# Kernel tuning notes

Measured on AMD Instinct MI355X. Metric: run time of the kernel, lower is better.

Reference implementation:

```python
import jax, jax.numpy as jnp
import numpy as np

B, S, H = 32, 4096, 768   # tuples, seq len, longformer hidden
N = 2048                  # total signals across all tuples (segments)
T = 16384                 # total pooled token indices (flattened ragged lists)
C = 32                    # char_size side features
D1, D2 = 512, 512         # MLP hidden dims


def setup_inputs() -> dict:
    key = jax.random.key(0)
    ks = jax.random.split(key, 9)
    hidden_states = jax.random.normal(ks[0], (B, S, H), dtype=jnp.float32)
    base_characteristics = jax.random.normal(ks[1], (N, C), dtype=jnp.float32)
    # MLP params: Linear(768+C,512) -> ReLU -> Linear(512,512) -> ReLU -> Linear(512,1) -> Sigmoid
    w1 = jax.random.normal(ks[2], (H + C, D1), dtype=jnp.float32) * 0.02
    b1 = jnp.zeros((D1,), dtype=jnp.float32)
    w2 = jax.random.normal(ks[3], (D1, D2), dtype=jnp.float32) * 0.02
    b2 = jnp.zeros((D2,), dtype=jnp.float32)
    w3 = jax.random.normal(ks[4], (D2, 1), dtype=jnp.float32) * 0.02
    b3 = jnp.zeros((1,), dtype=jnp.float32)
    # Flattened ragged pooling indices: token_indices index into flattened [B*S] tokens,
    # segment_ids map each index to its (tuple, signal) segment in [0, N).
    token_indices = jax.random.randint(ks[5], (T,), 0, B * S, dtype=jnp.int64)
    segment_ids = jnp.sort(jax.random.randint(ks[6], (T,), 0, N, dtype=jnp.int64))
    return {
        "hidden_states": hidden_states,
        "base_characteristics": base_characteristics,
        "w1": w1, "b1": b1, "w2": w2, "b2": b2, "w3": w3, "b3": b3,
        "token_indices": token_indices,
        "segment_ids": segment_ids,
    }


def reference(hidden_states, base_characteristics, w1, b1, w2, b2, w3, b3,
              token_indices, segment_ids):
    # Gather pooled token embeddings and segment-mean per signal.
    flat = hidden_states.reshape(-1, H)                       # [B*S, H]
    gathered = flat[token_indices]                            # [T, H]
    sums = jax.ops.segment_sum(gathered, segment_ids, num_segments=N)  # [N, H]
    counts = jax.ops.segment_sum(jnp.ones((T,), flat.dtype), segment_ids,
                                 num_segments=N)              # [N]
    pooled = sums / jnp.maximum(counts, 1.0)[:, None]         # mean pool per signal
    feats = jnp.concatenate([pooled, base_characteristics], axis=1)  # [N, H+C]
    h = jax.nn.relu(feats @ w1 + b1)
    h = jax.nn.relu(h @ w2 + b2)
    score = jax.nn.sigmoid(h @ w3 + b3)                       # [N, 1]
    return score.T                                            # [1, N], matches .T in torch
```

## Files before the change

kernel.cpp:

```cpp
#include <hip/hip_runtime.h>
#include <hip/hip_bf16.h>
#include <math.h>

#define HID   768
#define CHR   32
#define NSEG  2048
#define TTOK  16384
#define KF    800
#define D1    512
#define D2    512

typedef __hip_bfloat16 bf16;
typedef __attribute__((ext_vector_type(8))) short short8;
typedef __attribute__((ext_vector_type(4))) float floatx4;

__global__ __launch_bounds__(256) void pool_kernel(
    const float* __restrict__ hs,
    const float* __restrict__ basec,
    const int*   __restrict__ tok,
    const int*   __restrict__ seg,
    bf16*        __restrict__ feats)
{
    const int n   = blockIdx.x;
    const int tid = threadIdx.x;

    int lo;
    {
        int l = 0, r = TTOK;
        while (l < r) { int m = (l + r) >> 1; if (seg[m] < n) l = m + 1; else r = m; }
        lo = l;
    }
    int hi;
    {
        int l = lo, r = TTOK;
        while (l < r) { int m = (l + r) >> 1; if (seg[m] < n + 1) l = m + 1; else r = m; }
        hi = l;
    }

    float a0 = 0.f, a1 = 0.f, a2 = 0.f;
    for (int t = lo; t < hi; ++t) {
        const float* row = hs + (long)tok[t] * HID;
        a0 += row[tid];
        a1 += row[tid + 256];
        a2 += row[tid + 512];
    }
    const float inv = 1.0f / (float)((hi - lo) > 0 ? (hi - lo) : 1);
    bf16* frow = feats + (long)n * KF;
    frow[tid]       = __float2bfloat16(a0 * inv);
    frow[tid + 256] = __float2bfloat16(a1 * inv);
    frow[tid + 512] = __float2bfloat16(a2 * inv);
    if (tid < CHR) frow[HID + tid] = __float2bfloat16(basec[n * CHR + tid]);
}

__global__ __launch_bounds__(256) void transpose_convert(
    const float* __restrict__ in,
    bf16*        __restrict__ out,
    int K, int N)
{
    __shared__ float tile[32][33];
    const int k0 = blockIdx.x * 32;
    const int n0 = blockIdx.y * 32;
    const int tx = threadIdx.x & 31;
    const int ty = threadIdx.x >> 5;

    #pragma unroll
    for (int i = 0; i < 32; i += 8)
        tile[ty + i][tx] = in[(long)(k0 + ty + i) * N + (n0 + tx)];
    __syncthreads();
    #pragma unroll
    for (int i = 0; i < 32; i += 8)
        out[(long)(n0 + ty + i) * K + (k0 + tx)] = __float2bfloat16(tile[tx][ty + i]);
}

template <bool OUT_BF16>
__global__ __launch_bounds__(256) void gemm_bt(
    const bf16*  __restrict__ A,
    const bf16*  __restrict__ Bt,
    const float* __restrict__ bias,
    void*        __restrict__ Cout,
    int M, int N, int K)
{
    __shared__ short As[64 * 32];
    __shared__ short Bs[64 * 32];

    const int tid  = threadIdx.x;
    const int bm   = blockIdx.x * 64;
    const int bn   = blockIdx.y * 64;
    const int wave = tid >> 6;
    const int lane = tid & 63;
    const int wm   = wave >> 1;
    const int wn   = wave & 1;
    const int g    = lane >> 4;
    const int r    = lane & 15;

    const int srow = tid >> 2;
    const int sch  = tid & 3;
    const int sidx = srow * 32 + ((sch * 8) ^ ((srow & 3) << 3));

    const int nk = K / 32;

    floatx4 acc[2][2];
    #pragma unroll
    for (int i = 0; i < 2; ++i)
        #pragma unroll
        for (int j = 0; j < 2; ++j) acc[i][j] = (floatx4){0.f, 0.f, 0.f, 0.f};

    short8 areg = *(const short8*)(A  + (long)(bm + srow) * K + sch * 8);
    short8 breg = *(const short8*)(Bt + (long)(bn + srow) * K + sch * 8);
    *(short8*)(&As[sidx]) = areg;
    *(short8*)(&Bs[sidx]) = breg;

    for (int ks = 0; ks < nk; ++ks) {
        __syncthreads();

        if (ks + 1 < nk) {
            areg = *(const short8*)(A  + (long)(bm + srow) * K + (ks + 1) * 32 + sch * 8);
            breg = *(const short8*)(Bt + (long)(bn + srow) * K + (ks + 1) * 32 + sch * 8);
        }

        short8 af[2], bf[2];
        #pragma unroll
        for (int fm = 0; fm < 2; ++fm) {
            const int ar = wm * 32 + fm * 16 + r;
            af[fm] = *(const short8*)(&As[ar * 32 + ((g * 8) ^ ((ar & 3) << 3))]);
        }
        #pragma unroll
        for (int fn = 0; fn < 2; ++fn) {
            const int br = wn * 32 + fn * 16 + r;
            bf[fn] = *(const short8*)(&Bs[br * 32 + ((g * 8) ^ ((br & 3) << 3))]);
        }
        #pragma unroll
        for (int fm = 0; fm < 2; ++fm)
            #pragma unroll
            for (int fn = 0; fn < 2; ++fn)
                acc[fm][fn] = __builtin_amdgcn_mfma_f32_16x16x32_bf16(
                    af[fm], bf[fn], acc[fm][fn], 0, 0, 0);

        __syncthreads();

        if (ks + 1 < nk) {
            *(short8*)(&As[sidx]) = areg;
            *(short8*)(&Bs[sidx]) = breg;
        }
    }

    #pragma unroll
    for (int fm = 0; fm < 2; ++fm) {
        #pragma unroll
        for (int fn = 0; fn < 2; ++fn) {
            const int col = bn + wn * 32 + fn * 16 + r;
            const float bv = bias[col];
            #pragma unroll
            for (int j = 0; j < 4; ++j) {
                const int row = bm + wm * 32 + fm * 16 + g * 4 + j;
                float v = acc[fm][fn][j] + bv;
                v = fmaxf(v, 0.0f);
                if (OUT_BF16)
                    ((bf16*)Cout)[(long)row * N + col] = __float2bfloat16(v);
                else
                    ((float*)Cout)[(long)row * N + col] = v;
            }
        }
    }
}

__global__ __launch_bounds__(256) void final_kernel(
    const float* __restrict__ h2,
    const float* __restrict__ w3,
    const float* __restrict__ b3,
    float*       __restrict__ out)
{
    const int wave = threadIdx.x >> 6;
    const int lane = threadIdx.x & 63;
    const int n = blockIdx.x * 4 + wave;
    if (n >= NSEG) return;

    const float* row = h2 + (long)n * D2;
    float s = 0.f;
    #pragma unroll
    for (int i = 0; i < D2 / 64; ++i)
        s = fmaf(row[lane + i * 64], w3[lane + i * 64], s);

    #pragma unroll
    for (int off = 32; off > 0; off >>= 1)
        s += __shfl_xor(s, off, 64);

    if (lane == 0) {
        float x = s + b3[0];
        out[n] = 1.0f / (1.0f + expf(-x));
    }
}

extern "C" void kernel_launch(void* const* d_in, const int* in_sizes, int n_in,
                              void* d_out, int out_size, void* d_ws, size_t ws_size,
                              hipStream_t stream) {
    const float* hs    = (const float*)d_in[0];
    const float* basec = (const float*)d_in[1];
    const float* w1    = (const float*)d_in[2];
    const float* b1    = (const float*)d_in[3];
    const float* w2    = (const float*)d_in[4];
    const float* b2    = (const float*)d_in[5];
    const float* w3    = (const float*)d_in[6];
    const float* b3    = (const float*)d_in[7];
    const int*   tok   = (const int*)d_in[8];
    const int*   seg   = (const int*)d_in[9];
    float*       out   = (float*)d_out;

    char* ws = (char*)d_ws;
    bf16* feats = (bf16*)ws;  ws += (size_t)NSEG * KF * 2;
    bf16* w1t   = (bf16*)ws;  ws += (size_t)D1 * KF * 2;
    bf16* w2t   = (bf16*)ws;  ws += (size_t)D2 * D1 * 2;
    bf16* h1    = (bf16*)ws;  ws += (size_t)NSEG * D1 * 2;
    float* h2   = (float*)ws;

    pool_kernel<<<NSEG, 256, 0, stream>>>(hs, basec, tok, seg, feats);

    transpose_convert<<<dim3(KF / 32, D1 / 32), 256, 0, stream>>>(w1, w1t, KF, D1);
    transpose_convert<<<dim3(D1 / 32, D2 / 32), 256, 0, stream>>>(w2, w2t, D1, D2);

    gemm_bt<true ><<<dim3(NSEG / 64, D1 / 64), 256, 0, stream>>>(
        feats, w1t, b1, (void*)h1, NSEG, D1, KF);
    gemm_bt<false><<<dim3(NSEG / 64, D2 / 64), 256, 0, stream>>>(
        h1, w2t, b2, (void*)h2, NSEG, D2, D1);

    final_kernel<<<NSEG / 4, 256, 0, stream>>>(h2, w3, b3, out);
}
```

Measured before the change: 490.1 us.

## Fuse final dot into second GEMM, merge transposes, unroll pooling gather

The second GEMM epilogue now applies bias and ReLU, dots each row with w3 and atomically adds partial logits, so the fp32 h2 buffer is no longer written or re-read. A small sigmoid kernel finishes the output, and the pool kernel zeroes the logits. The two weight transposes are merged into one launch, and the pooling loop is unrolled by four to keep more gather loads in flight. Atomics add nondeterministic summation order, and there is still one extra kernel launch.

Result: no change. 485.8 us (-0.9%).

```diff
diff --git a/kernel.cpp b/kernel.cpp
--- a/kernel.cpp
+++ b/kernel.cpp
@@ -19,7 +19,8 @@
     const float* __restrict__ basec,
     const int*   __restrict__ tok,
     const int*   __restrict__ seg,
-    bf16*        __restrict__ feats)
+    bf16*        __restrict__ feats,
+    float*       __restrict__ logits)
 {
     const int n   = blockIdx.x;
     const int tid = threadIdx.x;
@@ -38,7 +39,21 @@
     }
 
     float a0 = 0.f, a1 = 0.f, a2 = 0.f;
-    for (int t = lo; t < hi; ++t) {
+    int t = lo;
+    for (; t + 4 <= hi; t += 4) {
+        const float* r0 = hs + (long)tok[t]     * HID;
+        const float* r1 = hs + (long)tok[t + 1] * HID;
+        const float* r2 = hs + (long)tok[t + 2] * HID;
+        const float* r3 = hs + (long)tok[t + 3] * HID;
+        float x0a = r0[tid], x0b = r0[tid + 256], x0c = r0[tid + 512];
+        float x1a = r1[tid], x1b = r1[tid + 256], x1c = r1[tid + 512];
+        float x2a = r2[tid], x2b = r2[tid + 256], x2c = r2[tid + 512];
+        float x3a = r3[tid], x3b = r3[tid + 256], x3c = r3[tid + 512];
+        a0 += (x0a + x1a) + (x2a + x3a);
+        a1 += (x0b + x1b) + (x2b + x3b);
+        a2 += (x0c + x1c) + (x2c + x3c);
+    }
+    for (; t < hi; ++t) {
         const float* row = hs + (long)tok[t] * HID;
         a0 += row[tid];
         a1 += row[tid + 256];
@@ -50,13 +65,20 @@
     frow[tid + 256] = __float2bfloat16(a1 * inv);
     frow[tid + 512] = __float2bfloat16(a2 * inv);
     if (tid < CHR) frow[HID + tid] = __float2bfloat16(basec[n * CHR + tid]);
-}
-
-__global__ __launch_bounds__(256) void transpose_convert(
-    const float* __restrict__ in,
-    bf16*        __restrict__ out,
-    int K, int N)
-{
+    if (tid == 0)  logits[n] = 0.0f;
+}
+
+__global__ __launch_bounds__(256) void transpose_both(
+    const float* __restrict__ w1, bf16* __restrict__ w1t,
+    const float* __restrict__ w2, bf16* __restrict__ w2t)
+{
+    const float* in; bf16* outp; int K, N;
+    if (blockIdx.z == 0) { in = w1; outp = w1t; K = KF; N = D1; }
+    else {
+        if (blockIdx.x >= D1 / 32) return;
+        in = w2; outp = w2t; K = D1; N = D2;
+    }
+
     __shared__ float tile[32][33];
     const int k0 = blockIdx.x * 32;
     const int n0 = blockIdx.y * 32;
@@ -69,15 +91,14 @@
     __syncthreads();
     #pragma unroll
     for (int i = 0; i < 32; i += 8)
-        out[(long)(n0 + ty + i) * K + (k0 + tx)] = __float2bfloat16(tile[tx][ty + i]);
-}
-
-template <bool OUT_BF16>
-__global__ __launch_bounds__(256) void gemm_bt(
+        outp[(long)(n0 + ty + i) * K + (k0 + tx)] = __float2bfloat16(tile[tx][ty + i]);
+}
+
+__global__ __launch_bounds__(256) void gemm_bt_relu(
     const bf16*  __restrict__ A,
     const bf16*  __restrict__ Bt,
     const float* __restrict__ bias,
-    void*        __restrict__ Cout,
+    bf16*        __restrict__ Cout,
     int M, int N, int K)
 {
     __shared__ short As[64 * 32];
@@ -118,7 +139,7 @@
             breg = *(const short8*)(Bt + (long)(bn + srow) * K + (ks + 1) * 32 + sch * 8);
         }
 
-        short8 af[2], bf[2];
+        short8 af[2], bfr[2];
         #pragma unroll
         for (int fm = 0; fm < 2; ++fm) {
             const int ar = wm * 32 + fm * 16 + r;
@@ -127,14 +148,14 @@
         #pragma unroll
         for (int fn = 0; fn < 2; ++fn) {
             const int br = wn * 32 + fn * 16 + r;
-            bf[fn] = *(const short8*)(&Bs[br * 32 + ((g * 8) ^ ((br & 3) << 3))]);
+            bfr[fn] = *(const short8*)(&Bs[br * 32 + ((g * 8) ^ ((br & 3) << 3))]);
         }
         #pragma unroll
         for (int fm = 0; fm < 2; ++fm)
             #pragma unroll
             for (int fn = 0; fn < 2; ++fn)
                 acc[fm][fn] = __builtin_amdgcn_mfma_f32_16x16x32_bf16(
-                    af[fm], bf[fn], acc[fm][fn], 0, 0, 0);
+                    af[fm], bfr[fn], acc[fm][fn], 0, 0, 0);
 
         __syncthreads();
 
@@ -153,40 +174,116 @@
             #pragma unroll
             for (int j = 0; j < 4; ++j) {
                 const int row = bm + wm * 32 + fm * 16 + g * 4 + j;
-                float v = acc[fm][fn][j] + bv;
-                v = fmaxf(v, 0.0f);
-                if (OUT_BF16)
-                    ((bf16*)Cout)[(long)row * N + col] = __float2bfloat16(v);
-                else
-                    ((float*)Cout)[(long)row * N + col] = v;
+                float v = fmaxf(acc[fm][fn][j] + bv, 0.0f);
+                Cout[(long)row * N + col] = __float2bfloat16(v);
             }
         }
     }
 }
 
-__global__ __launch_bounds__(256) void final_kernel(
-    const float* __restrict__ h2,
+__global__ __launch_bounds__(256) void gemm_bt_dot(
+    const bf16*  __restrict__ A,
+    const bf16*  __restrict__ Bt,
+    const float* __restrict__ bias,
     const float* __restrict__ w3,
+    float*       __restrict__ logits,
+    int M, int N, int K)
+{
+    __shared__ short As[64 * 32];
+    __shared__ short Bs[64 * 32];
+
+    const int tid  = threadIdx.x;
+    const int bm   = blockIdx.x * 64;
+    const int bn   = blockIdx.y * 64;
+    const int wave = tid >> 6;
+    const int lane = tid & 63;
+    const int wm   = wave >> 1;
+    const int wn   = wave & 1;
+    const int g    = lane >> 4;
+    const int r    = lane & 15;
+
+    const int srow = tid >> 2;
+    const int sch  = tid & 3;
+    const int sidx = srow * 32 + ((sch * 8) ^ ((srow & 3) << 3));
+
+    const int nk = K / 32;
+
+    floatx4 acc[2][2];
+    #pragma unroll
+    for (int i = 0; i < 2; ++i)
+        #pragma unroll
+        for (int j = 0; j < 2; ++j) acc[i][j] = (floatx4){0.f, 0.f, 0.f, 0.f};
+
+    short8 areg = *(const short8*)(A  + (long)(bm + srow) * K + sch * 8);
+    short8 breg = *(const short8*)(Bt + (long)(bn + srow) * K + sch * 8);
+    *(short8*)(&As[sidx]) = areg;
+    *(short8*)(&Bs[sidx]) = breg;
+
+    for (int ks = 0; ks < nk; ++ks) {
+        __syncthreads();
+
+        if (ks + 1 < nk) {
+            areg = *(const short8*)(A  + (long)(bm + srow) * K + (ks + 1) * 32 + sch * 8);
+            breg = *(const short8*)(Bt + (long)(bn + srow) * K + (ks + 1) * 32 + sch * 8);
+        }
+
+        short8 af[2], bfr[2];
+        #pragma unroll
+        for (int fm = 0; fm < 2; ++fm) {
+            const int ar = wm * 32 + fm * 16 + r;
+            af[fm] = *(const short8*)(&As[ar * 32 + ((g * 8) ^ ((ar & 3) << 3))]);
+        }
+        #pragma unroll
+        for (int fn = 0; fn < 2; ++fn) {
+            const int br = wn * 32 + fn * 16 + r;
+            bfr[fn] = *(const short8*)(&Bs[br * 32 + ((g * 8) ^ ((br & 3) << 3))]);
+        }
+        #pragma unroll
+        for (int fm = 0; fm < 2; ++fm)
+            #pragma unroll
+            for (int fn = 0; fn < 2; ++fn)
+                acc[fm][fn] = __builtin_amdgcn_mfma_f32_16x16x32_bf16(
+                    af[fm], bfr[fn], acc[fm][fn], 0, 0, 0);
+
+        __syncthreads();
+
+        if (ks + 1 < nk) {
+            *(short8*)(&As[sidx]) = areg;
+            *(short8*)(&Bs[sidx]) = breg;
+        }
+    }
+
+    #pragma unroll
+    for (int fm = 0; fm < 2; ++fm) {
+        #pragma unroll
+        for (int j = 0; j < 4; ++j) {
+            float s = 0.f;
+            #pragma unroll
+            for (int fn = 0; fn < 2; ++fn) {
+                const int col = bn + wn * 32 + fn * 16 + r;
+                float v = fmaxf(acc[fm][fn][j] + bias[col], 0.0f);
+                s = fmaf(v, w3[col], s);
+            }
+            s += __shfl_xor(s, 1, 64);
+            s += __shfl_xor(s, 2, 64);
+            s += __shfl_xor(s, 4, 64);
+            s += __shfl_xor(s, 8, 64);
+            if (r == 0) {
+                const int row = bm + wm * 32 + fm * 16 + g * 4 + j;
+                atomicAdd(&logits[row], s);
+            }
+        }
+    }
+}
+
+__global__ __launch_bounds__(256) void sigmoid_kernel(
+    const float* __restrict__ logits,
     const float* __restrict__ b3,
     float*       __restrict__ out)
 {
-    const int wave = threadIdx.x >> 6;
-    const int lane = threadIdx.x & 63;
-    const int n = blockIdx.x * 4 + wave;
-    if (n >= NSEG) return;
-
-    const float* row = h2 + (long)n * D2;
-    float s = 0.f;
-    #pragma unroll
-    for (int i = 0; i < D2 / 64; ++i)
-        s = fmaf(row[lane + i * 64], w3[lane + i * 64], s);
-
-    #pragma unroll
-    for (int off = 32; off > 0; off >>= 1)
-        s += __shfl_xor(s, off, 64);
-
-    if (lane == 0) {
-        float x = s + b3[0];
+    const int n = blockIdx.x * 256 + threadIdx.x;
+    if (n < NSEG) {
+        float x = logits[n] + b3[0];
         out[n] = 1.0f / (1.0f + expf(-x));
     }
 }
@@ -207,21 +304,21 @@
     float*       out   = (float*)d_out;
 
     char* ws = (char*)d_ws;
-    bf16* feats = (bf16*)ws;  ws += (size_t)NSEG * KF * 2;
-    bf16* w1t   = (bf16*)ws;  ws += (size_t)D1 * KF * 2;
-    bf16* w2t   = (bf16*)ws;  ws += (size_t)D2 * D1 * 2;
-    bf16* h1    = (bf16*)ws;  ws += (size_t)NSEG * D1 * 2;
-    float* h2   = (float*)ws;
-
-    pool_kernel<<<NSEG, 256, 0, stream>>>(hs, basec, tok, seg, feats);
-
-    transpose_convert<<<dim3(KF / 32, D1 / 32), 256, 0, stream>>>(w1, w1t, KF, D1);
-    transpose_convert<<<dim3(D1 / 32, D2 / 32), 256, 0, stream>>>(w2, w2t, D1, D2);
-
-    gemm_bt<true ><<<dim3(NSEG / 64, D1 / 64), 256, 0, stream>>>(
-        feats, w1t, b1, (void*)h1, NSEG, D1, KF);
-    gemm_bt<false><<<dim3(NSEG / 64, D2 / 64), 256, 0, stream>>>(
-        h1, w2t, b2, (void*)h2, NSEG, D2, D1);
-
-    final_kernel<<<NSEG / 4, 256, 0, stream>>>(h2, w3, b3, out);
-}
+    bf16*  feats  = (bf16*)ws;   ws += (size_t)NSEG * KF * 2;
+    bf16*  w1t    = (bf16*)ws;   ws += (size_t)D1 * KF * 2;
+    bf16*  w2t    = (bf16*)ws;   ws += (size_t)D2 * D1 * 2;
+    bf16*  h1     = (bf16*)ws;   ws += (size_t)NSEG * D1 * 2;
+    float* logits = (float*)ws;
+
+    pool_kernel<<<NSEG, 256, 0, stream>>>(hs, basec, tok, seg, feats, logits);
+
+    transpose_both<<<dim3(KF / 32, D1 / 32, 2), 256, 0, stream>>>(w1, w1t, w2, w2t);
+
+    gemm_bt_relu<<<dim3(NSEG / 64, D1 / 64), 256, 0, stream>>>(
+        feats, w1t, b1, h1, NSEG, D1, KF);
+
+    gemm_bt_dot<<<dim3(NSEG / 64, D2 / 64), 256, 0, stream>>>(
+        h1, w2t, b2, w3, logits, NSEG, D2, D1);
+
+    sigmoid_kernel<<<NSEG / 256, 256, 0, stream>>>(logits, b3, out);
+}
```
